# Optimization experiments

Hardware: AMD Instinct MI355X
Metric: run time of the kernel (lower is better)

The kernel has to match this reference:

```python
import jax, jax.numpy as jnp
import numpy as np

B, Q, K, DQ, DK, H, DV = 4, 512, 512, 512, 512, 256, 512


def setup_inputs() -> dict:
    key = jax.random.key(0)
    ks = jax.random.split(key, 9)
    return {
        "query": jax.random.normal(ks[0], (B, Q, DQ), dtype=jnp.float32),
        "key": jax.random.normal(ks[1], (B, K, DK), dtype=jnp.float32),
        "value": jax.random.normal(ks[2], (B, K, DV), dtype=jnp.float32),
        "Wq": jax.random.normal(ks[3], (DQ, H), dtype=jnp.float32) / np.sqrt(DQ),
        "bq": jax.random.normal(ks[4], (H,), dtype=jnp.float32) * 0.01,
        "Wk": jax.random.normal(ks[5], (DK, H), dtype=jnp.float32) / np.sqrt(DK),
        "bk": jax.random.normal(ks[6], (H,), dtype=jnp.float32) * 0.01,
        "wv": jax.random.normal(ks[7], (H,), dtype=jnp.float32) / np.sqrt(H),
        "bv": jax.random.normal(ks[8], (), dtype=jnp.float32) * 0.01,
    }


def reference(query, key, value, Wq, bq, Wk, bk, wv, bv):
    # Projections: [B,Q,H] and [B,K,H]
    q = jnp.einsum("bqd,dh->bqh", query, Wq) + bq
    k = jnp.einsum("bkd,dh->bkh", key, Wk) + bk
    # Broadcast add + tanh: [B,Q,K,H] (the large intermediate)
    feat = jnp.tanh(q[:, :, None, :] + k[:, None, :, :])
    # Linear-to-scalar score: [B,Q,K]
    score = jnp.einsum("bqkh,h->bqk", feat, wv) + bv
    attention_weight = jax.nn.softmax(score, axis=-1)
    # Dropout is identity at eval; weighted sum over keys: [B,Q,DV]
    context = jnp.einsum("bqk,bkd->bqd", attention_weight, value)
    return (context, attention_weight)
```

## Files before the change

### kernel.cpp

```cpp
#include <hip/hip_runtime.h>
#include <hip/hip_bf16.h>

#define B_ 4
#define Q_ 512
#define K_ 512
#define DQ_ 512
#define H_ 256
#define DV_ 512

#define SC2 2.8853900817779268f

typedef unsigned short u16;
typedef short bf16x8 __attribute__((ext_vector_type(8)));
typedef float f32x4 __attribute__((ext_vector_type(4)));
typedef float f32x2 __attribute__((ext_vector_type(2)));
typedef unsigned short u16x4 __attribute__((ext_vector_type(4)));

__device__ __forceinline__ unsigned bsplit(float a) {
    unsigned u  = __float_as_uint(a);
    unsigned hi = (u + 0x7FFFu + ((u >> 16) & 1u)) >> 16;
    float hf = __uint_as_float(hi << 16);
    float l  = a - hf;
    unsigned ul = __float_as_uint(l);
    unsigned lo = (ul + 0x7FFFu + ((ul >> 16) & 1u)) >> 16;
    return (hi << 16) | lo;
}

__device__ __forceinline__ void gld16(const void* g, void* l) {
    __builtin_amdgcn_global_load_lds(
        (const __attribute__((address_space(1))) unsigned int*)g,
        (__attribute__((address_space(3))) unsigned int*)l, 16, 0, 0);
}

__device__ __forceinline__ void pair_acc(
    f32x2 Eq0, f32x2 Eq1, float ek0, float ek1,
    float w0, float w1, float w01, f32x2& acc)
{
    f32x2 e0 = Eq0 * (f32x2){ek0, ek0};
    f32x2 e1 = Eq1 * (f32x2){ek1, ek1};
    f32x2 s  = e0 + e1;
    f32x2 den = __builtin_elementwise_fma(e0, e1, s);
    den = den + (f32x2){1.f, 1.f};
    f32x2 num = __builtin_elementwise_fma(e1, (f32x2){w0, w0}, (f32x2){w01, w01});
    num = __builtin_elementwise_fma(e0, (f32x2){w1, w1}, num);
    f32x2 r = {__builtin_amdgcn_rcpf(den.x), __builtin_amdgcn_rcpf(den.y)};
    acc = __builtin_elementwise_fma(num, r, acc);
}

__global__ __launch_bounds__(256) void prep_all(
    const float* __restrict__ query, const float* __restrict__ key,
    const float* __restrict__ Wq, const float* __restrict__ Wk,
    const float* __restrict__ value,
    u16* __restrict__ qA_hi, u16* __restrict__ qA_lo,
    u16* __restrict__ WT_hi, u16* __restrict__ WT_lo,
    u16* __restrict__ vT_hi, u16* __restrict__ vT_lo)
{
    const int bx  = blockIdx.x;
    const int tid = threadIdx.x;

    if (bx < 2048) {
        const int z = bx >> 10;
        const float* src = z ? key : query;
        u16* dh = qA_hi + (long long)z * 1048576;
        u16* dl = qA_lo + (long long)z * 1048576;
        long long i4 = (long long)(bx & 1023) * 256 + tid;
        float4 v = ((const float4*)src)[i4];
        unsigned a = bsplit(v.x), b = bsplit(v.y), c = bsplit(v.z), d = bsplit(v.w);
        u16x4 h4 = {(u16)(a >> 16), (u16)(b >> 16), (u16)(c >> 16), (u16)(d >> 16)};
        u16x4 l4 = {(u16)(a & 0xFFFF), (u16)(b & 0xFFFF), (u16)(c & 0xFFFF), (u16)(d & 0xFFFF)};
        *(u16x4*)(dh + i4 * 4) = h4;
        *(u16x4*)(dl + i4 * 4) = l4;
        return;
    }

    __shared__ float t[32][33];
    const int flat = bx - 2048;
    const int z  = flat >> 8;
    const int rem = flat & 255;
    const int gx = rem & 15, gy = rem >> 4;
    const int x = tid & 31, y = tid >> 5;
    const float* src; u16 *dh, *dl; int C;
    if (z < 2) {
        if (gy >= 8) return;
        src = z ? Wk : Wq; C = 256;
        dh = WT_hi + (long long)z * 131072;
        dl = WT_lo + (long long)z * 131072;
    } else {
        src = value + (long long)(z - 2) * 262144; C = 512;
        dh = vT_hi + (long long)(z - 2) * 262144;
        dl = vT_lo + (long long)(z - 2) * 262144;
    }
    const int r0 = gx * 32, c0 = gy * 32;
    #pragma unroll
    for (int i = 0; i < 32; i += 8)
        t[y + i][x] = src[(long long)(r0 + y + i) * C + c0 + x];
    __syncthreads();
    {
        const int r = tid >> 3, c = tid & 7;
        unsigned p0 = bsplit(t[4 * c + 0][r]);
        unsigned p1 = bsplit(t[4 * c + 1][r]);
        unsigned p2 = bsplit(t[4 * c + 2][r]);
        unsigned p3 = bsplit(t[4 * c + 3][r]);
        long long o = (long long)(c0 + r) * 512 + r0 + 4 * c;
        u16x4 h4 = {(u16)(p0 >> 16), (u16)(p1 >> 16), (u16)(p2 >> 16), (u16)(p3 >> 16)};
        u16x4 l4 = {(u16)(p0 & 0xFFFF), (u16)(p1 & 0xFFFF), (u16)(p2 & 0xFFFF), (u16)(p3 & 0xFFFF)};
        *(u16x4*)(dh + o) = h4;
        *(u16x4*)(dl + o) = l4;
    }
}

__global__ __launch_bounds__(256) void mfma_gemm(
    const u16* __restrict__ Ah0, const u16* __restrict__ Al0,
    const u16* __restrict__ Bh0, const u16* __restrict__ Bl0,
    const float* __restrict__ biasq, const float* __restrict__ biask,
    float* __restrict__ outp, int mode, int Kd,
    long long sA, long long sB, long long sO)
{
    const int z = blockIdx.z;
    const u16* Ah = Ah0 + z * sA;
    const u16* Al = Al0 + z * sA;
    const u16* Bh = Bh0 + z * sB;
    const u16* Bl = Bl0 + z * sB;

    const int m0 = blockIdx.x * 64;
    const int n0 = blockIdx.y * 64;

    __shared__ u16 AhS[2][64 * 64], AlS[2][64 * 64], BhS[2][64 * 64], BlS[2][64 * 64];

    const int tid = threadIdx.x;
    const int lane = tid & 63, w = tid >> 6;
    const int wr = w >> 1, wc = w & 1;
    const int lrow = lane & 15, lgrp = lane >> 4;

    f32x4 acc[2][2] = {};

    const int idx0 = tid, idx1 = tid + 256;
    const int row0 = idx0 >> 3, u0 = idx0 & 7;
    const int row1 = idx1 >> 3, u1 = idx1 & 7;
    const long long goA0 = (long long)(m0 + row0) * Kd + ((u0 ^ (row0 & 7)) << 3);
    const long long goA1 = (long long)(m0 + row1) * Kd + ((u1 ^ (row1 & 7)) << 3);
    const long long goB0 = (long long)(n0 + row0) * Kd + ((u0 ^ (row0 & 7)) << 3);
    const long long goB1 = (long long)(n0 + row1) * Kd + ((u1 ^ (row1 & 7)) << 3);

#define STAGE(BI, K0) do {                                    \
        gld16(Ah + goA0 + (K0), &AhS[BI][idx0 * 8]);          \
        gld16(Al + goA0 + (K0), &AlS[BI][idx0 * 8]);          \
        gld16(Bh + goB0 + (K0), &BhS[BI][idx0 * 8]);          \
        gld16(Bl + goB0 + (K0), &BlS[BI][idx0 * 8]);          \
        gld16(Ah + goA1 + (K0), &AhS[BI][idx1 * 8]);          \
        gld16(Al + goA1 + (K0), &AlS[BI][idx1 * 8]);          \
        gld16(Bh + goB1 + (K0), &BhS[BI][idx1 * 8]);          \
        gld16(Bl + goB1 + (K0), &BlS[BI][idx1 * 8]);          \
    } while (0)

    STAGE(0, 0);
    __syncthreads();

    int cur = 0;
    for (int k0 = 0; k0 < Kd; k0 += 64) {
        if (k0 + 64 < Kd) STAGE(cur ^ 1, k0 + 64);

        #pragma unroll
        for (int kk = 0; kk < 2; ++kk) {
            bf16x8 ah[2], al[2], bh[2], bl[2];
            #pragma unroll
            for (int f = 0; f < 2; ++f) {
                int ar = wr * 32 + f * 16 + lrow;
                int au = (kk * 4 + lgrp) ^ (ar & 7);
                ah[f] = *(const bf16x8*)(&AhS[cur][ar * 64 + au * 8]);
                al[f] = *(const bf16x8*)(&AlS[cur][ar * 64 + au * 8]);
                int br = wc * 32 + f * 16 + lrow;
                int bu = (kk * 4 + lgrp) ^ (br & 7);
                bh[f] = *(const bf16x8*)(&BhS[cur][br * 64 + bu * 8]);
                bl[f] = *(const bf16x8*)(&BlS[cur][br * 64 + bu * 8]);
            }
            #pragma unroll
            for (int fm = 0; fm < 2; ++fm)
                #pragma unroll
                for (int fn = 0; fn < 2; ++fn) {
                    acc[fm][fn] = __builtin_amdgcn_mfma_f32_16x16x32_bf16(ah[fm], bh[fn], acc[fm][fn], 0, 0, 0);
                    acc[fm][fn] = __builtin_amdgcn_mfma_f32_16x16x32_bf16(ah[fm], bl[fn], acc[fm][fn], 0, 0, 0);
                    acc[fm][fn] = __builtin_amdgcn_mfma_f32_16x16x32_bf16(al[fm], bh[fn], acc[fm][fn], 0, 0, 0);
                }
        }
        __syncthreads();
        cur ^= 1;
    }
#undef STAGE

    if (mode == 0) {
        const float* bs = z ? biask : biasq;
        #pragma unroll
        for (int fm = 0; fm < 2; ++fm)
            #pragma unroll
            for (int fn = 0; fn < 2; ++fn)
                #pragma unroll
                for (int r = 0; r < 4; ++r) {
                    int m = m0 + wr * 32 + fm * 16 + lgrp * 4 + r;
                    int n = n0 + wc * 32 + fn * 16 + lrow;
                    float v = __builtin_amdgcn_exp2f((acc[fm][fn][r] + bs[n]) * SC2);
                    if (z == 0) {
                        outp[(((long long)(m >> 2) * H_ + n) << 2) + (m & 3)] = v;
                    } else {
                        int bb = m >> 9, k = m & 511;
                        outp[sO + (((long long)(bb * 64 + (n >> 2)) * 512 + k) << 2) + (n & 3)] = v;
                    }
                }
    } else {
        float* C = outp + (long long)z * sO;
        #pragma unroll
        for (int fm = 0; fm < 2; ++fm)
            #pragma unroll
            for (int fn = 0; fn < 2; ++fn)
                #pragma unroll
                for (int r = 0; r < 4; ++r) {
                    int m = m0 + wr * 32 + fm * 16 + lgrp * 4 + r;
                    int n = n0 + wc * 32 + fn * 16 + lrow;
                    C[(long long)m * DV_ + n] = acc[fm][fn][r];
                }
    }
}

#define QT 8

__global__ __launch_bounds__(1024) void score_softmax(
    const float* __restrict__ qp4E,
    const float* __restrict__ kT4E,
    const float* __restrict__ wv,
    float* __restrict__ attn_out,
    u16* __restrict__ aB_hi, u16* __restrict__ aB_lo)
{
    const int b   = blockIdx.y;
    const int q0  = blockIdx.x * QT;
    const int tid = threadIdx.x;
    const int k16 = tid & 255;
    const int qtr = tid >> 8;
    const int lane = tid & 63;

    __shared__ float lq[H_][8];
    __shared__ float lwp[H_ / 2][4];
    __shared__ float pacc[3][2][256][8];
    __shared__ float red[4][QT];

    if (tid < 256) {
        const float4* qA = (const float4*)qp4E + ((long long)(b * (Q_ / 4) + 2 * blockIdx.x)) * H_;
        *(float4*)&lq[tid][0] = qA[tid];
    } else if (tid < 512) {
        int h = tid - 256;
        const float4* qB = (const float4*)qp4E + ((long long)(b * (Q_ / 4) + 2 * blockIdx.x + 1)) * H_;
        *(float4*)&lq[h][4] = qB[h];
    } else if (tid < 512 + 128) {
        int p = tid - 512;
        float w0 = wv[2 * p], w1 = wv[2 * p + 1];
        lwp[p][0] = w0; lwp[p][1] = w1; lwp[p][2] = w0 + w1; lwp[p][3] = 0.f;
    }
    __syncthreads();

    f32x2 aA[4] = {{0.f,0.f},{0.f,0.f},{0.f,0.f},{0.f,0.f}};
    f32x2 aB[4] = {{0.f,0.f},{0.f,0.f},{0.f,0.f},{0.f,0.f}};
    const float4* kvec = (const float4*)kT4E + (long long)b * (H_ / 4) * K_ + k16;
    const int g0 = qtr * 16;

    float4 kA = kvec[(long long)g0 * K_];
    float4 kB = kvec[(long long)g0 * K_ + 256];
    #pragma unroll 2
    for (int gi = 0; gi < 16; ++gi) {
        const int g = g0 + gi;
        float4 kAc = kA, kBc = kB;
        if (gi < 15) {
            kA = kvec[(long long)(g + 1) * K_];
            kB = kvec[(long long)(g + 1) * K_ + 256];
        }
        float4 wp0 = *(const float4*)&lwp[(g << 1) + 0][0];
        float4 wp1 = *(const float4*)&lwp[(g << 1) + 1][0];

        float4 qa0 = *(const float4*)&lq[(g << 2) + 0][0];
        float4 qb0 = *(const float4*)&lq[(g << 2) + 0][4];
        float4 qa1 = *(const float4*)&lq[(g << 2) + 1][0];
        float4 qb1 = *(const float4*)&lq[(g << 2) + 1][4];
        float4 qa2 = *(const float4*)&lq[(g << 2) + 2][0];
        float4 qb2 = *(const float4*)&lq[(g << 2) + 2][4];
        float4 qa3 = *(const float4*)&lq[(g << 2) + 3][0];
        float4 qb3 = *(const float4*)&lq[(g << 2) + 3][4];

        f32x2 q0p[4] = {{qa0.x,qa0.y},{qa0.z,qa0.w},{qb0.x,qb0.y},{qb0.z,qb0.w}};
        f32x2 q1p[4] = {{qa1.x,qa1.y},{qa1.z,qa1.w},{qb1.x,qb1.y},{qb1.z,qb1.w}};
        f32x2 q2p[4] = {{qa2.x,qa2.y},{qa2.z,qa2.w},{qb2.x,qb2.y},{qb2.z,qb2.w}};
        f32x2 q3p[4] = {{qa3.x,qa3.y},{qa3.z,qa3.w},{qb3.x,qb3.y},{qb3.z,qb3.w}};

        #pragma unroll
        for (int qp = 0; qp < 4; ++qp) {
            pair_acc(q0p[qp], q1p[qp], kAc.x, kAc.y, wp0.x, wp0.y, wp0.z, aA[qp]);
            pair_acc(q2p[qp], q3p[qp], kAc.z, kAc.w, wp1.x, wp1.y, wp1.z, aA[qp]);
            pair_acc(q0p[qp], q1p[qp], kBc.x, kBc.y, wp0.x, wp0.y, wp0.z, aB[qp]);
            pair_acc(q2p[qp], q3p[qp], kBc.z, kBc.w, wp1.x, wp1.y, wp1.z, aB[qp]);
        }
    }

    if (qtr) {
        float4 vA0 = make_float4(aA[0].x, aA[0].y, aA[1].x, aA[1].y);
        float4 vA1 = make_float4(aA[2].x, aA[2].y, aA[3].x, aA[3].y);
        float4 vB0 = make_float4(aB[0].x, aB[0].y, aB[1].x, aB[1].y);
        float4 vB1 = make_float4(aB[2].x, aB[2].y, aB[3].x, aB[3].y);
        *(float4*)&pacc[qtr - 1][0][k16][0] = vA0;
        *(float4*)&pacc[qtr - 1][0][k16][4] = vA1;
        *(float4*)&pacc[qtr - 1][1][k16][0] = vB0;
        *(float4*)&pacc[qtr - 1][1][k16][4] = vB1;
    }
    __syncthreads();

    float e[2][QT];
    if (!qtr) {
        float s[2][QT];
        #pragma unroll
        for (int qp = 0; qp < 4; ++qp) {
            s[0][2*qp]   = aA[qp].x;
            s[0][2*qp+1] = aA[qp].y;
            s[1][2*qp]   = aB[qp].x;
            s[1][2*qp+1] = aB[qp].y;
        }
        #pragma unroll
        for (int o = 0; o < 3; ++o) {
            #pragma unroll
            for (int kk = 0; kk < 2; ++kk) {
                float4 t0 = *(const float4*)&pacc[o][kk][k16][0];
                float4 t1 = *(const float4*)&pacc[o][kk][k16][4];
                s[kk][0] += t0.x; s[kk][1] += t0.y; s[kk][2] += t0.z; s[kk][3] += t0.w;
                s[kk][4] += t1.x; s[kk][5] += t1.y; s[kk][6] += t1.z; s[kk][7] += t1.w;
            }
        }
        #pragma unroll
        for (int kk = 0; kk < 2; ++kk)
            #pragma unroll
            for (int qq = 0; qq < QT; ++qq)
                e[kk][qq] = __builtin_amdgcn_exp2f(-SC2 * s[kk][qq]);
        #pragma unroll
        for (int qq = 0; qq < QT; ++qq) {
            float v = e[0][qq] + e[1][qq];
            #pragma unroll
            for (int off = 32; off; off >>= 1) v += __shfl_xor(v, off);
            if (lane == 0) red[tid >> 6][qq] = v;
        }
    }
    __syncthreads();
    if (!qtr) {
        #pragma unroll
        for (int qq = 0; qq < QT; ++qq) {
            float v = red[0][qq] + red[1][qq] + red[2][qq] + red[3][qq];
            float rv = __builtin_amdgcn_rcpf(v);
            #pragma unroll
            for (int kk = 0; kk < 2; ++kk) {
                float a = e[kk][qq] * rv;
                long long o = (long long)(b * Q_ + q0 + qq) * K_ + k16 + kk * 256;
                attn_out[o] = a;
                unsigned p = bsplit(a);
                aB_hi[o] = (u16)(p >> 16);
                aB_lo[o] = (u16)(p & 0xFFFF);
            }
        }
    }
}

extern "C" void kernel_launch(void* const* d_in, const int* in_sizes, int n_in,
                              void* d_out, int out_size, void* d_ws, size_t ws_size,
                              hipStream_t stream) {
    const float* query = (const float*)d_in[0];
    const float* key   = (const float*)d_in[1];
    const float* value = (const float*)d_in[2];
    const float* Wq    = (const float*)d_in[3];
    const float* bq    = (const float*)d_in[4];
    const float* Wk    = (const float*)d_in[5];
    const float* bk    = (const float*)d_in[6];
    const float* wv    = (const float*)d_in[7];

    float* out = (float*)d_out;
    float* ctx_out  = out;
    float* attn_out = out + (size_t)B_ * Q_ * DV_;

    float* ws   = (float*)d_ws;
    float* qp4  = ws;
    float* kT4  = qp4 + 524288;
    u16* qA_hi  = (u16*)(kT4 + 524288);
    u16* kA_hi  = qA_hi + 1048576;
    u16* qA_lo  = kA_hi + 1048576;
    u16* kA_lo  = qA_lo + 1048576;
    u16* WqT_hi = kA_lo + 1048576;
    u16* WkT_hi = WqT_hi + 131072;
    u16* WqT_lo = WkT_hi + 131072;
    u16* WkT_lo = WqT_lo + 131072;
    u16* vT_hi  = WkT_lo + 131072;
    u16* vT_lo  = vT_hi + 1048576;
    u16* aB_hi  = vT_lo + 1048576;
    u16* aB_lo  = aB_hi + 1048576;
    (void)qA_lo; (void)WqT_lo; (void)n_in; (void)ws_size; (void)in_sizes; (void)out_size;

    hipLaunchKernelGGL(prep_all, dim3(3584), dim3(256), 0, stream,
                       query, key, Wq, Wk, value,
                       qA_hi, qA_lo, WqT_hi, WqT_lo, vT_hi, vT_lo);

    hipLaunchKernelGGL(mfma_gemm, dim3(32, 4, 2), dim3(256), 0, stream,
                       qA_hi, qA_lo, WqT_hi, WqT_lo, bq, bk, qp4, 0, 512,
                       (long long)1048576, (long long)131072, (long long)524288);

    hipLaunchKernelGGL(score_softmax, dim3(Q_ / QT, B_), dim3(1024), 0, stream,
                       qp4, kT4, wv, attn_out, aB_hi, aB_lo);

    hipLaunchKernelGGL(mfma_gemm, dim3(8, 8, 4), dim3(256), 0, stream,
                       aB_hi, aB_lo, vT_hi, vT_lo, (const float*)nullptr, (const float*)nullptr,
                       ctx_out, 2, 512,
                       (long long)262144, (long long)262144, (long long)262144);
}
```

Measured before the change: 61.31 us.

## Split-K both GEMMs in two halves with separate combine kernels

```diff
diff --git a/kernel.cpp b/kernel.cpp
--- a/kernel.cpp
+++ b/kernel.cpp
@@ -112,15 +112,18 @@
 __global__ __launch_bounds__(256) void mfma_gemm(
     const u16* __restrict__ Ah0, const u16* __restrict__ Al0,
     const u16* __restrict__ Bh0, const u16* __restrict__ Bl0,
-    const float* __restrict__ biasq, const float* __restrict__ biask,
-    float* __restrict__ outp, int mode, int Kd,
+    float* __restrict__ psum, int Kd, int Nout,
     long long sA, long long sB, long long sO)
 {
     const int z = blockIdx.z;
-    const u16* Ah = Ah0 + z * sA;
-    const u16* Al = Al0 + z * sA;
-    const u16* Bh = Bh0 + z * sB;
-    const u16* Bl = Bl0 + z * sB;
+    const int pair = z >> 1, half = z & 1;
+    const int kStart = half * (Kd >> 1);
+    const int kLen   = Kd >> 1;
+    const u16* Ah = Ah0 + pair * sA;
+    const u16* Al = Al0 + pair * sA;
+    const u16* Bh = Bh0 + pair * sB;
+    const u16* Bl = Bl0 + pair * sB;
+    float* out = psum + (long long)z * sO;
 
     const int m0 = blockIdx.x * 64;
     const int n0 = blockIdx.y * 64;
@@ -137,10 +140,10 @@
     const int idx0 = tid, idx1 = tid + 256;
     const int row0 = idx0 >> 3, u0 = idx0 & 7;
     const int row1 = idx1 >> 3, u1 = idx1 & 7;
-    const long long goA0 = (long long)(m0 + row0) * Kd + ((u0 ^ (row0 & 7)) << 3);
-    const long long goA1 = (long long)(m0 + row1) * Kd + ((u1 ^ (row1 & 7)) << 3);
-    const long long goB0 = (long long)(n0 + row0) * Kd + ((u0 ^ (row0 & 7)) << 3);
-    const long long goB1 = (long long)(n0 + row1) * Kd + ((u1 ^ (row1 & 7)) << 3);
+    const long long goA0 = (long long)(m0 + row0) * Kd + kStart + ((u0 ^ (row0 & 7)) << 3);
+    const long long goA1 = (long long)(m0 + row1) * Kd + kStart + ((u1 ^ (row1 & 7)) << 3);
+    const long long goB0 = (long long)(n0 + row0) * Kd + kStart + ((u0 ^ (row0 & 7)) << 3);
+    const long long goB1 = (long long)(n0 + row1) * Kd + kStart + ((u1 ^ (row1 & 7)) << 3);
 
 #define STAGE(BI, K0) do {                                    \
         gld16(Ah + goA0 + (K0), &AhS[BI][idx0 * 8]);          \
@@ -157,8 +160,8 @@
     __syncthreads();
 
     int cur = 0;
-    for (int k0 = 0; k0 < Kd; k0 += 64) {
-        if (k0 + 64 < Kd) STAGE(cur ^ 1, k0 + 64);
+    for (int k0 = 0; k0 < kLen; k0 += 64) {
+        if (k0 + 64 < kLen) STAGE(cur ^ 1, k0 + 64);
 
         #pragma unroll
         for (int kk = 0; kk < 2; ++kk) {
@@ -188,37 +191,59 @@
     }
 #undef STAGE
 
-    if (mode == 0) {
-        const float* bs = z ? biask : biasq;
-        #pragma unroll
-        for (int fm = 0; fm < 2; ++fm)
-            #pragma unroll
-            for (int fn = 0; fn < 2; ++fn)
-                #pragma unroll
-                for (int r = 0; r < 4; ++r) {
-                    int m = m0 + wr * 32 + fm * 16 + lgrp * 4 + r;
-                    int n = n0 + wc * 32 + fn * 16 + lrow;
-                    float v = __builtin_amdgcn_exp2f((acc[fm][fn][r] + bs[n]) * SC2);
-                    if (z == 0) {
-                        outp[(((long long)(m >> 2) * H_ + n) << 2) + (m & 3)] = v;
-                    } else {
-                        int bb = m >> 9, k = m & 511;
-                        outp[sO + (((long long)(bb * 64 + (n >> 2)) * 512 + k) << 2) + (n & 3)] = v;
-                    }
-                }
+    #pragma unroll
+    for (int fm = 0; fm < 2; ++fm)
+        #pragma unroll
+        for (int fn = 0; fn < 2; ++fn)
+            #pragma unroll
+            for (int r = 0; r < 4; ++r) {
+                int m = m0 + wr * 32 + fm * 16 + lgrp * 4 + r;
+                int n = n0 + wc * 32 + fn * 16 + lrow;
+                out[(long long)m * Nout + n] = acc[fm][fn][r];
+            }
+}
+
+__global__ __launch_bounds__(256) void proj_combine(
+    const float* __restrict__ psum,
+    const float* __restrict__ bq, const float* __restrict__ bk,
+    float* __restrict__ qp4E, float* __restrict__ kT4E)
+{
+    const int idx = blockIdx.x * 256 + threadIdx.x;
+    const int op  = idx >> 17;
+    const int rem = idx & 131071;
+    const int m = rem >> 6, n = (rem & 63) * 4;
+    const float* bs = op ? bk : bq;
+    float4 p0 = *(const float4*)&psum[(long long)(op * 2 + 0) * 524288 + (long long)m * 256 + n];
+    float4 p1 = *(const float4*)&psum[(long long)(op * 2 + 1) * 524288 + (long long)m * 256 + n];
+    float4 b4 = *(const float4*)&bs[n];
+    float v0 = __builtin_amdgcn_exp2f((p0.x + p1.x + b4.x) * SC2);
+    float v1 = __builtin_amdgcn_exp2f((p0.y + p1.y + b4.y) * SC2);
+    float v2 = __builtin_amdgcn_exp2f((p0.z + p1.z + b4.z) * SC2);
+    float v3 = __builtin_amdgcn_exp2f((p0.w + p1.w + b4.w) * SC2);
+    if (op == 0) {
+        long long base = ((long long)(m >> 2) * H_ + n) * 4 + (m & 3);
+        qp4E[base + 0]  = v0;
+        qp4E[base + 4]  = v1;
+        qp4E[base + 8]  = v2;
+        qp4E[base + 12] = v3;
     } else {
-        float* C = outp + (long long)z * sO;
-        #pragma unroll
-        for (int fm = 0; fm < 2; ++fm)
-            #pragma unroll
-            for (int fn = 0; fn < 2; ++fn)
-                #pragma unroll
-                for (int r = 0; r < 4; ++r) {
-                    int m = m0 + wr * 32 + fm * 16 + lgrp * 4 + r;
-                    int n = n0 + wc * 32 + fn * 16 + lrow;
-                    C[(long long)m * DV_ + n] = acc[fm][fn][r];
-                }
-    }
+        int bb = m >> 9, kk = m & 511;
+        *(float4*)&kT4E[((long long)(bb * 64 + (n >> 2)) * 512 + kk) << 2] =
+            make_float4(v0, v1, v2, v3);
+    }
+}
+
+__global__ __launch_bounds__(256) void pv_combine(
+    const float* __restrict__ psum, float* __restrict__ ctx)
+{
+    const int idx = blockIdx.x * 256 + threadIdx.x;
+    const int batch = idx >> 16;
+    const int rem = idx & 65535;
+    const float4* p0 = (const float4*)&psum[(long long)(batch * 2 + 0) * 262144];
+    const float4* p1 = (const float4*)&psum[(long long)(batch * 2 + 1) * 262144];
+    float4 a = p0[rem], b = p1[rem];
+    ((float4*)&ctx[(long long)batch * 262144])[rem] =
+        make_float4(a.x + b.x, a.y + b.y, a.z + b.z, a.w + b.w);
 }
 
 #define QT 8
@@ -392,21 +417,25 @@
     u16* vT_lo  = vT_hi + 1048576;
     u16* aB_hi  = vT_lo + 1048576;
     u16* aB_lo  = aB_hi + 1048576;
+    float* psum = (float*)(aB_lo + 1048576);
     (void)qA_lo; (void)WqT_lo; (void)n_in; (void)ws_size; (void)in_sizes; (void)out_size;
 
     hipLaunchKernelGGL(prep_all, dim3(3584), dim3(256), 0, stream,
                        query, key, Wq, Wk, value,
                        qA_hi, qA_lo, WqT_hi, WqT_lo, vT_hi, vT_lo);
 
-    hipLaunchKernelGGL(mfma_gemm, dim3(32, 4, 2), dim3(256), 0, stream,
-                       qA_hi, qA_lo, WqT_hi, WqT_lo, bq, bk, qp4, 0, 512,
+    hipLaunchKernelGGL(mfma_gemm, dim3(32, 4, 4), dim3(256), 0, stream,
+                       qA_hi, qA_lo, WqT_hi, WqT_lo, psum, 512, 256,
                        (long long)1048576, (long long)131072, (long long)524288);
+    hipLaunchKernelGGL(proj_combine, dim3(1024), dim3(256), 0, stream,
+                       psum, bq, bk, qp4, kT4);
 
     hipLaunchKernelGGL(score_softmax, dim3(Q_ / QT, B_), dim3(1024), 0, stream,
                        qp4, kT4, wv, attn_out, aB_hi, aB_lo);
 
-    hipLaunchKernelGGL(mfma_gemm, dim3(8, 8, 4), dim3(256), 0, stream,
-                       aB_hi, aB_lo, vT_hi, vT_lo, (const float*)nullptr, (const float*)nullptr,
-                       ctx_out, 2, 512,
+    hipLaunchKernelGGL(mfma_gemm, dim3(8, 8, 8), dim3(256), 0, stream,
+                       aB_hi, aB_lo, vT_hi, vT_lo, psum, 512, 512,
                        (long long)262144, (long long)262144, (long long)262144);
-}
+    hipLaunchKernelGGL(pv_combine, dim3(1024), dim3(256), 0, stream,
+                       psum, ctx_out);
+}
```

Result: slower. 67.52 us (+10.1%).
